# Kernel tuning notes

Measured on AMD Instinct MI355X. Metric: run time of the kernel, lower is better.

Reference implementation:

```python
import jax, jax.numpy as jnp
import numpy as np

NEG_INF = -1e9  # additive mask value for masked softmax


def setup_inputs() -> dict:
    key = jax.random.key(0)
    k1, k2, k3, k4, k5 = jax.random.split(key, 5)
    bz, rv_num, rv_len, in_feat, out_feat = 32, 10, 128, 300, 128
    seq_a = jax.random.normal(k1, (bz, rv_num, rv_len, in_feat), dtype=jnp.float32)
    seq_b = jax.random.normal(k2, (bz, rv_num, rv_len, in_feat), dtype=jnp.float32)
    mask_a = jax.random.randint(k3, (bz, rv_num, rv_len), 0, 2, dtype=jnp.int32)
    mask_b = jax.random.randint(k4, (bz, rv_num, rv_len), 0, 2, dtype=jnp.int32)
    # guarantee at least one valid position per review (avoid fully-masked rows)
    mask_a = mask_a.at[:, :, 0].set(1)
    mask_b = mask_b.at[:, :, 0].set(1)
    # FC transform params (xavier-normal-ish weight, zero bias)
    W = jax.random.normal(k5, (in_feat, out_feat), dtype=jnp.float32) * (2.0 / np.sqrt(in_feat + out_feat))
    b = jnp.zeros((out_feat,), dtype=jnp.float32)
    return {"seq_a": seq_a, "seq_b": seq_b, "mask_a": mask_a, "mask_b": mask_b, "W": W, "b": b}


def _masked_softmax(scores, mask):
    # scores: [N, L], mask: [N, L] in {0,1}
    logits = jnp.where(mask > 0, scores, NEG_INF)
    return jax.nn.softmax(logits, axis=-1)


def reference(seq_a, seq_b, mask_a, mask_b, W, b):
    bz, rv_num, rv_len, _ = seq_a.shape
    hdim = W.shape[1]
    N = bz * rv_num          # flattened batch of reviews
    M = rv_num * rv_len      # all tokens on the other side

    # FC + ReLU feature transform
    ta = jax.nn.relu(jnp.einsum('bnld,dh->bnlh', seq_a, W) + b)
    tb = jax.nn.relu(jnp.einsum('bnld,dh->bnlh', seq_b, W) + b)

    sa = ta.reshape(N, rv_len, hdim)
    sb = tb.reshape(N, rv_len, hdim)
    # expand: each review attends over ALL tokens of the other sequence in its sample
    ea = jnp.broadcast_to(ta.reshape(bz, 1, M, hdim), (bz, rv_num, M, hdim)).reshape(N, M, hdim)
    eb = jnp.broadcast_to(tb.reshape(bz, 1, M, hdim), (bz, rv_num, M, hdim)).reshape(N, M, hdim)

    # DOT interaction (no scale): affinity [N, rv_len, M]
    atob_aff = jnp.einsum('nld,nmd->nlm', sa, eb)
    btoa_aff = jnp.einsum('nld,nmd->nlm', sb, ea)

    # MEAN pooling over the other-sequence axis
    atob_scores = atob_aff.mean(axis=-1)  # [N, rv_len]
    btoa_scores = btoa_aff.mean(axis=-1)

    ma = mask_a.reshape(N, rv_len)
    mb = mask_b.reshape(N, rv_len)
    atob_w = _masked_softmax(atob_scores, ma)
    btoa_w = _masked_softmax(btoa_scores, mb)

    a_out = jnp.einsum('nl,nld->nd', atob_w, sa)
    b_out = jnp.einsum('nl,nld->nd', btoa_w, sb)
    return (a_out, b_out, atob_w, btoa_w)
```

## Files before the change

### kernel.cpp

```cpp
#include <hip/hip_runtime.h>
#include <hip/hip_bf16.h>


#define K_FEAT 300
#define H 128
#define NTOK 40960
#define NREV 320
#define TOK_PER_SAMPLE 1280
#define TM 64
#define FC_BLKS_PER_SIDE 640
#define FC_BLKS_PER_SAMPLE 20
#define LDA 40
#define NCHUNK 10
#define WFRAG_ELEMS (NCHUNK * 4 * 4 * 64 * 8)

typedef __attribute__((ext_vector_type(8))) short bf16x8;
typedef __attribute__((ext_vector_type(4))) float f32x4;
typedef unsigned short u16;
typedef unsigned int u32;

static __device__ __forceinline__ u16 f2bf(float x) {
    u32 u = __float_as_uint(x);
    return (u16)((u + 0x7fffu + ((u >> 16) & 1u)) >> 16);
}
static __device__ __forceinline__ float bf2f(u16 s) {
    return __uint_as_float(((u32)s) << 16);
}

__global__ void wsplit_kernel(const float* __restrict__ W, u16* __restrict__ Wfrag)
{
    int i = blockIdx.x * 256 + threadIdx.x;
    if (i >= WFRAG_ELEMS) return;
    int j    = i & 7;
    int lane = (i >> 3) & 63;
    int frag = (i >> 9) & 3;
    int wave = (i >> 11) & 3;
    int c    = i >> 13;
    int nn = lane & 15, quad = lane >> 4;
    int t2 = frag >> 1, part = frag & 1;
    int h = (2 * wave + t2) * 16 + nn;
    int k = c * 32 + quad * 8 + j;
    float w = (k < K_FEAT) ? W[(size_t)k * H + h] : 0.f;
    u16 hi = f2bf(w);
    Wfrag[i] = part ? f2bf(w - bf2f(hi)) : hi;
}

__global__ __launch_bounds__(256, 5) void fc_mfma_kernel(
    const float* __restrict__ seq_a, const float* __restrict__ seq_b,
    const u16* __restrict__ Wfrag, const float* __restrict__ bias,
    u16* __restrict__ ta, u16* __restrict__ tb,
    float* __restrict__ psum_a, float* __restrict__ psum_b)
{
    __shared__ u16 Ah_s[2][TM * LDA];
    __shared__ u16 Al_s[2][TM * LDA];
    __shared__ float bias_s[H];

    int blk = blockIdx.x;
    const float* seq; u16* outp; float* psum;
    if (blk < FC_BLKS_PER_SIDE) { seq = seq_a; outp = ta; psum = psum_a; }
    else { seq = seq_b; outp = tb; psum = psum_b; blk -= FC_BLKS_PER_SIDE; }

    const int tid = threadIdx.x;
    const int tok0 = blk * TM;
    const int wave = tid >> 6;
    const int lane = tid & 63;
    const int nn = lane & 15;
    const int quad = lane >> 4;

    if (tid < H) bias_s[tid] = bias[tid];

    const int st_t = tid >> 3;
    const int st_j = tid & 7;

    f32x4 acc[4][2];
#pragma unroll
    for (int m = 0; m < 4; ++m) {
        acc[m][0] = (f32x4){0.f, 0.f, 0.f, 0.f};
        acc[m][1] = (f32x4){0.f, 0.f, 0.f, 0.f};
    }

    float4 pf[2];
#pragma unroll
    for (int it = 0; it < 2; ++it) {
        int t = st_t + it * 32;
        pf[it] = *(const float4*)&seq[(size_t)(tok0 + t) * K_FEAT + 4 * st_j];
    }
#pragma unroll
    for (int it = 0; it < 2; ++it) {
        int t = st_t + it * 32;
        float4 v = pf[it];
        u16 h0 = f2bf(v.x), h1 = f2bf(v.y), h2 = f2bf(v.z), h3 = f2bf(v.w);
        uint2 hp, lp;
        hp.x = (u32)h0 | ((u32)h1 << 16);
        hp.y = (u32)h2 | ((u32)h3 << 16);
        lp.x = (u32)f2bf(v.x - bf2f(h0)) | ((u32)f2bf(v.y - bf2f(h1)) << 16);
        lp.y = (u32)f2bf(v.z - bf2f(h2)) | ((u32)f2bf(v.w - bf2f(h3)) << 16);
        *(uint2*)&Ah_s[0][t * LDA + 4 * st_j] = hp;
        *(uint2*)&Al_s[0][t * LDA + 4 * st_j] = lp;
    }
    __syncthreads();

#pragma unroll
    for (int c = 0; c < NCHUNK; ++c) {
        const int cur = c & 1;
        if (c < NCHUNK - 1) {
#pragma unroll
            for (int it = 0; it < 2; ++it) {
                int t = st_t + it * 32;
                int kk = (c + 1) * 32 + 4 * st_j;
                pf[it] = make_float4(0.f, 0.f, 0.f, 0.f);
                if (kk + 4 <= K_FEAT)
                    pf[it] = *(const float4*)&seq[(size_t)(tok0 + t) * K_FEAT + kk];
            }
        }
        const u16* wf = Wfrag + (size_t)(c * 4 + wave) * 2048;
        bf16x8 bh0 = *(const bf16x8*)&wf[0 * 512 + lane * 8];
        bf16x8 bl0 = *(const bf16x8*)&wf[1 * 512 + lane * 8];
        bf16x8 bh1 = *(const bf16x8*)&wf[2 * 512 + lane * 8];
        bf16x8 bl1 = *(const bf16x8*)&wf[3 * 512 + lane * 8];
#pragma unroll
        for (int m = 0; m < 4; ++m) {
            bf16x8 a_hi = *(const bf16x8*)&Ah_s[cur][(m * 16 + nn) * LDA + quad * 8];
            bf16x8 a_lo = *(const bf16x8*)&Al_s[cur][(m * 16 + nn) * LDA + quad * 8];
            acc[m][0] = __builtin_amdgcn_mfma_f32_16x16x32_bf16(bh0, a_hi, acc[m][0], 0, 0, 0);
            acc[m][0] = __builtin_amdgcn_mfma_f32_16x16x32_bf16(bl0, a_hi, acc[m][0], 0, 0, 0);
            acc[m][0] = __builtin_amdgcn_mfma_f32_16x16x32_bf16(bh0, a_lo, acc[m][0], 0, 0, 0);
            acc[m][1] = __builtin_amdgcn_mfma_f32_16x16x32_bf16(bh1, a_hi, acc[m][1], 0, 0, 0);
            acc[m][1] = __builtin_amdgcn_mfma_f32_16x16x32_bf16(bl1, a_hi, acc[m][1], 0, 0, 0);
            acc[m][1] = __builtin_amdgcn_mfma_f32_16x16x32_bf16(bh1, a_lo, acc[m][1], 0, 0, 0);
        }
        if (c < NCHUNK - 1) {
#pragma unroll
            for (int it = 0; it < 2; ++it) {
                int t = st_t + it * 32;
                float4 v = pf[it];
                u16 h0 = f2bf(v.x), h1 = f2bf(v.y), h2 = f2bf(v.z), h3 = f2bf(v.w);
                uint2 hp, lp;
                hp.x = (u32)h0 | ((u32)h1 << 16);
                hp.y = (u32)h2 | ((u32)h3 << 16);
                lp.x = (u32)f2bf(v.x - bf2f(h0)) | ((u32)f2bf(v.y - bf2f(h1)) << 16);
                lp.y = (u32)f2bf(v.z - bf2f(h2)) | ((u32)f2bf(v.w - bf2f(h3)) << 16);
                *(uint2*)&Ah_s[cur ^ 1][t * LDA + 4 * st_j] = hp;
                *(uint2*)&Al_s[cur ^ 1][t * LDA + 4 * st_j] = lp;
            }
            __syncthreads();
        }
    }

#pragma unroll
    for (int ht = 0; ht < 2; ++ht) {
        int h0 = (2 * wave + ht) * 16 + quad * 4;
        float4 bb = *(const float4*)&bias_s[h0];
        float fs[4] = {0.f, 0.f, 0.f, 0.f};
#pragma unroll
        for (int tt = 0; tt < 4; ++tt) {
            int tok = tok0 + tt * 16 + nn;
            float v0 = fmaxf(acc[tt][ht][0] + bb.x, 0.f);
            float v1 = fmaxf(acc[tt][ht][1] + bb.y, 0.f);
            float v2 = fmaxf(acc[tt][ht][2] + bb.z, 0.f);
            float v3 = fmaxf(acc[tt][ht][3] + bb.w, 0.f);
            fs[0] += v0; fs[1] += v1; fs[2] += v2; fs[3] += v3;
            uint2 p;
            p.x = (u32)f2bf(v0) | ((u32)f2bf(v1) << 16);
            p.y = (u32)f2bf(v2) | ((u32)f2bf(v3) << 16);
            *(uint2*)&outp[(size_t)tok * H + h0] = p;
        }
#pragma unroll
        for (int r = 0; r < 4; ++r) {
            fs[r] += __shfl_xor(fs[r], 1);
            fs[r] += __shfl_xor(fs[r], 2);
            fs[r] += __shfl_xor(fs[r], 4);
            fs[r] += __shfl_xor(fs[r], 8);
        }
        if (nn == 0) {
#pragma unroll
            for (int r = 0; r < 4; ++r)
                psum[(size_t)blk * H + h0 + r] = fs[r];
        }
    }
}

__global__ __launch_bounds__(512) void attn_kernel(
    const u16* __restrict__ ta, const u16* __restrict__ tb,
    const int* __restrict__ mask_a, const int* __restrict__ mask_b,
    const float* __restrict__ psum_a, const float* __restrict__ psum_b,
    float* __restrict__ out)
{
    int n = blockIdx.x;
    int side = 0;
    if (n >= NREV) { side = 1; n -= NREV; }

    const u16* t = side ? tb : ta;
    const int* mask = side ? mask_b : mask_a;
    const float* psum_o = side ? psum_a : psum_b;
    float* out_vec = out + (side ? NREV * H : 0);
    float* out_w = out + 2 * NREV * H + (side ? NREV * H : 0);

    int sample = n / 10;
    int tid = threadIdx.x;

    __shared__ float score_part[128 * 17];
    __shared__ float mean_s[128];
    __shared__ float w_s[128];
    __shared__ float red[8];
    __shared__ float part_out[32 * 128];

    if (tid < 128) {
        float s = 0.f;
        const float* pb = psum_o + (size_t)sample * FC_BLKS_PER_SAMPLE * H + tid;
#pragma unroll
        for (int i = 0; i < FC_BLKS_PER_SAMPLE; ++i) s += pb[(size_t)i * H];
        mean_s[tid] = s * (1.0f / (float)TOK_PER_SAMPLE);
    }
    __syncthreads();

    const u16* rowbase = t + (size_t)n * 128 * H;

#pragma unroll
    for (int i = 0; i < 4; ++i) {
        int q = tid + 512 * i;
        int r = q >> 4;
        int c8 = q & 15;
        uint4 v = *(const uint4*)&rowbase[r * H + c8 * 8];
        const float* m = &mean_s[c8 * 8];
        float p = 0.f;
        p += bf2f((u16)(v.x & 0xffff)) * m[0];
        p += bf2f((u16)(v.x >> 16)) * m[1];
        p += bf2f((u16)(v.y & 0xffff)) * m[2];
        p += bf2f((u16)(v.y >> 16)) * m[3];
        p += bf2f((u16)(v.z & 0xffff)) * m[4];
        p += bf2f((u16)(v.z >> 16)) * m[5];
        p += bf2f((u16)(v.w & 0xffff)) * m[6];
        p += bf2f((u16)(v.w >> 16)) * m[7];
        score_part[r * 17 + c8] = p;
    }
    __syncthreads();

    float logit = -1e9f;
    if (tid < 128) {
        float s = 0.f;
#pragma unroll
        for (int j = 0; j < 16; ++j) s += score_part[tid * 17 + j];
        int mv = mask[n * 128 + tid];
        logit = (mv > 0) ? s : -1e9f;
    }

    float mx = logit;
    for (int off = 32; off > 0; off >>= 1) mx = fmaxf(mx, __shfl_xor(mx, off));
    if ((tid & 63) == 0) red[tid >> 6] = mx;
    __syncthreads();
    mx = red[0];
#pragma unroll
    for (int rr = 1; rr < 8; ++rr) mx = fmaxf(mx, red[rr]);
    __syncthreads();

    float e = __expf(logit - mx);
    float ssum = e;
    for (int off = 32; off > 0; off >>= 1) ssum += __shfl_xor(ssum, off);
    if ((tid & 63) == 0) red[tid >> 6] = ssum;
    __syncthreads();
    ssum = 0.f;
#pragma unroll
    for (int rr = 0; rr < 8; ++rr) ssum += red[rr];

    float w = e / ssum;
    if (tid < 128) {
        w_s[tid] = w;
        out_w[n * 128 + tid] = w;
    }
    __syncthreads();

    int c8 = tid & 15;
    int lp = tid >> 4;
    float o[8] = {0.f, 0.f, 0.f, 0.f, 0.f, 0.f, 0.f, 0.f};
#pragma unroll
    for (int k = 0; k < 4; ++k) {
        int l = k * 32 + lp;
        float wl = w_s[l];
        uint4 v = *(const uint4*)&rowbase[l * H + c8 * 8];
        o[0] = fmaf(wl, bf2f((u16)(v.x & 0xffff)), o[0]);
        o[1] = fmaf(wl, bf2f((u16)(v.x >> 16)), o[1]);
        o[2] = fmaf(wl, bf2f((u16)(v.y & 0xffff)), o[2]);
        o[3] = fmaf(wl, bf2f((u16)(v.y >> 16)), o[3]);
        o[4] = fmaf(wl, bf2f((u16)(v.z & 0xffff)), o[4]);
        o[5] = fmaf(wl, bf2f((u16)(v.z >> 16)), o[5]);
        o[6] = fmaf(wl, bf2f((u16)(v.w & 0xffff)), o[6]);
        o[7] = fmaf(wl, bf2f((u16)(v.w >> 16)), o[7]);
    }
    *(float4*)&part_out[lp * 128 + c8 * 8] = make_float4(o[0], o[1], o[2], o[3]);
    *(float4*)&part_out[lp * 128 + c8 * 8 + 4] = make_float4(o[4], o[5], o[6], o[7]);
    __syncthreads();
    if (tid < 128) {
        float s = 0.f;
#pragma unroll
        for (int p = 0; p < 32; ++p) s += part_out[p * 128 + tid];
        out_vec[n * 128 + tid] = s;
    }
}

extern "C" void kernel_launch(void* const* d_in, const int* in_sizes, int n_in,
                              void* d_out, int out_size, void* d_ws, size_t ws_size,
                              hipStream_t stream)
{
    const float* seq_a = (const float*)d_in[0];
    const float* seq_b = (const float*)d_in[1];
    const int* mask_a = (const int*)d_in[2];
    const int* mask_b = (const int*)d_in[3];
    const float* W = (const float*)d_in[4];
    const float* bias = (const float*)d_in[5];
    float* out = (float*)d_out;

    u16* ta = (u16*)d_ws;
    u16* tb = ta + (size_t)NTOK * H;
    float* psum_a = (float*)(tb + (size_t)NTOK * H);
    float* psum_b = psum_a + FC_BLKS_PER_SIDE * H;
    u16* Wfrag = (u16*)(psum_b + FC_BLKS_PER_SIDE * H);

    wsplit_kernel<<<(WFRAG_ELEMS + 255) / 256, 256, 0, stream>>>(W, Wfrag);
    fc_mfma_kernel<<<2 * FC_BLKS_PER_SIDE, 256, 0, stream>>>(seq_a, seq_b, Wfrag, bias, ta, tb, psum_a, psum_b);
    attn_kernel<<<640, 512, 0, stream>>>(ta, tb, mask_a, mask_b, psum_a, psum_b, out);
}
```

Measured before the change: 150.6 us.

## Store A tiles in MFMA fragment order and prefetch two chunks ahead

Shared-memory A tiles are now written in the exact per-lane MFMA fragment layout, so each lane reads its operand as one contiguous 16-byte load instead of a padded row-strided access. Each thread stages 8 consecutive k values as 16-byte stores rather than 4-element 8-byte stores. Global loads are issued two chunks ahead using two register sets, which gives more latency hiding at the cost of extra VGPRs under the 5-wave launch bound.

New measurement: 152.8 us. About the same (+1.5%).

```diff
diff --git a/kernel.cpp b/kernel.cpp
--- a/kernel.cpp
+++ b/kernel.cpp
@@ -10,7 +10,6 @@
 #define TM 64
 #define FC_BLKS_PER_SIDE 640
 #define FC_BLKS_PER_SAMPLE 20
-#define LDA 40
 #define NCHUNK 10
 #define WFRAG_ELEMS (NCHUNK * 4 * 4 * 64 * 8)
 
@@ -45,14 +44,29 @@
     Wfrag[i] = part ? f2bf(w - bf2f(hi)) : hi;
 }
 
+static __device__ __forceinline__ void cvt_pack(const float4 a, const float4 b,
+                                                uint4& hp, uint4& lp)
+{
+    u16 h0 = f2bf(a.x), h1 = f2bf(a.y), h2 = f2bf(a.z), h3 = f2bf(a.w);
+    u16 h4 = f2bf(b.x), h5 = f2bf(b.y), h6 = f2bf(b.z), h7 = f2bf(b.w);
+    hp.x = (u32)h0 | ((u32)h1 << 16);
+    hp.y = (u32)h2 | ((u32)h3 << 16);
+    hp.z = (u32)h4 | ((u32)h5 << 16);
+    hp.w = (u32)h6 | ((u32)h7 << 16);
+    lp.x = (u32)f2bf(a.x - bf2f(h0)) | ((u32)f2bf(a.y - bf2f(h1)) << 16);
+    lp.y = (u32)f2bf(a.z - bf2f(h2)) | ((u32)f2bf(a.w - bf2f(h3)) << 16);
+    lp.z = (u32)f2bf(b.x - bf2f(h4)) | ((u32)f2bf(b.y - bf2f(h5)) << 16);
+    lp.w = (u32)f2bf(b.z - bf2f(h6)) | ((u32)f2bf(b.w - bf2f(h7)) << 16);
+}
+
 __global__ __launch_bounds__(256, 5) void fc_mfma_kernel(
     const float* __restrict__ seq_a, const float* __restrict__ seq_b,
     const u16* __restrict__ Wfrag, const float* __restrict__ bias,
     u16* __restrict__ ta, u16* __restrict__ tb,
     float* __restrict__ psum_a, float* __restrict__ psum_b)
 {
-    __shared__ u16 Ah_s[2][TM * LDA];
-    __shared__ u16 Al_s[2][TM * LDA];
+    __shared__ __align__(16) u16 Ah_s[2][4 * 512];
+    __shared__ __align__(16) u16 Al_s[2][4 * 512];
     __shared__ float bias_s[H];
 
     int blk = blockIdx.x;
@@ -69,8 +83,10 @@
 
     if (tid < H) bias_s[tid] = bias[tid];
 
-    const int st_t = tid >> 3;
-    const int st_j = tid & 7;
+    const int st_tok = tid >> 2;
+    const int st_q = tid & 3;
+    const float* srow = seq + (size_t)(tok0 + st_tok) * K_FEAT + st_q * 8;
+    const int stg = (st_tok >> 4) * 512 + ((st_q << 4) + (st_tok & 15)) * 8;
 
     f32x4 acc[4][2];
 #pragma unroll
@@ -79,39 +95,33 @@
         acc[m][1] = (f32x4){0.f, 0.f, 0.f, 0.f};
     }
 
-    float4 pf[2];
-#pragma unroll
-    for (int it = 0; it < 2; ++it) {
-        int t = st_t + it * 32;
-        pf[it] = *(const float4*)&seq[(size_t)(tok0 + t) * K_FEAT + 4 * st_j];
-    }
-#pragma unroll
-    for (int it = 0; it < 2; ++it) {
-        int t = st_t + it * 32;
-        float4 v = pf[it];
-        u16 h0 = f2bf(v.x), h1 = f2bf(v.y), h2 = f2bf(v.z), h3 = f2bf(v.w);
-        uint2 hp, lp;
-        hp.x = (u32)h0 | ((u32)h1 << 16);
-        hp.y = (u32)h2 | ((u32)h3 << 16);
-        lp.x = (u32)f2bf(v.x - bf2f(h0)) | ((u32)f2bf(v.y - bf2f(h1)) << 16);
-        lp.y = (u32)f2bf(v.z - bf2f(h2)) | ((u32)f2bf(v.w - bf2f(h3)) << 16);
-        *(uint2*)&Ah_s[0][t * LDA + 4 * st_j] = hp;
-        *(uint2*)&Al_s[0][t * LDA + 4 * st_j] = lp;
-    }
+#define LOADC(cc, x0, x1) do {                                  \
+        int kchk = (cc) * 32 + st_q * 8;                        \
+        x0 = make_float4(0.f, 0.f, 0.f, 0.f);                   \
+        x1 = make_float4(0.f, 0.f, 0.f, 0.f);                   \
+        if (kchk + 4 <= K_FEAT) x0 = *(const float4*)(srow + (cc) * 32);     \
+        if (kchk + 8 <= K_FEAT) x1 = *(const float4*)(srow + (cc) * 32 + 4); \
+    } while (0)
+
+#define STOREC(bufi, x0, x1) do {                               \
+        uint4 hp, lp;                                           \
+        cvt_pack(x0, x1, hp, lp);                               \
+        *(uint4*)&Ah_s[bufi][stg] = hp;                         \
+        *(uint4*)&Al_s[bufi][stg] = lp;                         \
+    } while (0)
+
+    float4 a0, a1, b0, b1;
+    LOADC(0, a0, a1);
+    LOADC(1, b0, b1);
+    STOREC(0, a0, a1);
     __syncthreads();
 
 #pragma unroll
     for (int c = 0; c < NCHUNK; ++c) {
         const int cur = c & 1;
-        if (c < NCHUNK - 1) {
-#pragma unroll
-            for (int it = 0; it < 2; ++it) {
-                int t = st_t + it * 32;
-                int kk = (c + 1) * 32 + 4 * st_j;
-                pf[it] = make_float4(0.f, 0.f, 0.f, 0.f);
-                if (kk + 4 <= K_FEAT)
-                    pf[it] = *(const float4*)&seq[(size_t)(tok0 + t) * K_FEAT + kk];
-            }
+        if (c + 2 < NCHUNK) {
+            if ((c & 1) == 0) { LOADC(c + 2, a0, a1); }
+            else              { LOADC(c + 2, b0, b1); }
         }
         const u16* wf = Wfrag + (size_t)(c * 4 + wave) * 2048;
         bf16x8 bh0 = *(const bf16x8*)&wf[0 * 512 + lane * 8];
@@ -120,8 +130,8 @@
         bf16x8 bl1 = *(const bf16x8*)&wf[3 * 512 + lane * 8];
 #pragma unroll
         for (int m = 0; m < 4; ++m) {
-            bf16x8 a_hi = *(const bf16x8*)&Ah_s[cur][(m * 16 + nn) * LDA + quad * 8];
-            bf16x8 a_lo = *(const bf16x8*)&Al_s[cur][(m * 16 + nn) * LDA + quad * 8];
+            bf16x8 a_hi = *(const bf16x8*)&Ah_s[cur][m * 512 + lane * 8];
+            bf16x8 a_lo = *(const bf16x8*)&Al_s[cur][m * 512 + lane * 8];
             acc[m][0] = __builtin_amdgcn_mfma_f32_16x16x32_bf16(bh0, a_hi, acc[m][0], 0, 0, 0);
             acc[m][0] = __builtin_amdgcn_mfma_f32_16x16x32_bf16(bl0, a_hi, acc[m][0], 0, 0, 0);
             acc[m][0] = __builtin_amdgcn_mfma_f32_16x16x32_bf16(bh0, a_lo, acc[m][0], 0, 0, 0);
@@ -129,23 +139,14 @@
             acc[m][1] = __builtin_amdgcn_mfma_f32_16x16x32_bf16(bl1, a_hi, acc[m][1], 0, 0, 0);
             acc[m][1] = __builtin_amdgcn_mfma_f32_16x16x32_bf16(bh1, a_lo, acc[m][1], 0, 0, 0);
         }
-        if (c < NCHUNK - 1) {
-#pragma unroll
-            for (int it = 0; it < 2; ++it) {
-                int t = st_t + it * 32;
-                float4 v = pf[it];
-                u16 h0 = f2bf(v.x), h1 = f2bf(v.y), h2 = f2bf(v.z), h3 = f2bf(v.w);
-                uint2 hp, lp;
-                hp.x = (u32)h0 | ((u32)h1 << 16);
-                hp.y = (u32)h2 | ((u32)h3 << 16);
-                lp.x = (u32)f2bf(v.x - bf2f(h0)) | ((u32)f2bf(v.y - bf2f(h1)) << 16);
-                lp.y = (u32)f2bf(v.z - bf2f(h2)) | ((u32)f2bf(v.w - bf2f(h3)) << 16);
-                *(uint2*)&Ah_s[cur ^ 1][t * LDA + 4 * st_j] = hp;
-                *(uint2*)&Al_s[cur ^ 1][t * LDA + 4 * st_j] = lp;
-            }
+        if (c + 1 < NCHUNK) {
+            if ((c & 1) == 0) { STOREC(cur ^ 1, b0, b1); }
+            else              { STOREC(cur ^ 1, a0, a1); }
             __syncthreads();
         }
     }
+#undef LOADC
+#undef STOREC
 
 #pragma unroll
     for (int ht = 0; ht < 2; ++ht) {
```
